# Kernel optimization log

Hardware: AMD Instinct MI355X
Metric: run time of the kernel (lower is better)

Reference implementation:

```python
import jax, jax.numpy as jnp
import numpy as np

B, S, C, H = 256, 512, 64, 128  # batch, seq_len, input channels, LSTM hidden


def setup_inputs() -> dict:
    key = jax.random.key(0)
    ks = jax.random.split(key, 9)
    s = 1.0 / np.sqrt(H)  # torch nn.LSTM init: U(-1/sqrt(H), 1/sqrt(H))
    u = lambda k, shape: jax.random.uniform(k, shape, jnp.float32, -s, s)
    return {
        "x": jax.random.normal(ks[0], (B, S, C), jnp.float32),
        # layer 0 (input size C)
        "Wih0": u(ks[1], (4 * H, C)),
        "Whh0": u(ks[2], (4 * H, H)),
        "bih0": u(ks[3], (4 * H,)),
        "bhh0": u(ks[4], (4 * H,)),
        # layer 1 (input size H)
        "Wih1": u(ks[5], (4 * H, H)),
        "Whh1": u(ks[6], (4 * H, H)),
        "bih1": u(ks[7], (4 * H,)),
        "bhh1": u(ks[8], (4 * H,)),
    }


def _lstm_layer(x, Wih, Whh, bih, bhh):
    """x: (S, B, in) -> outputs h_t for all t: (S, B, H). Torch gate order i,f,g,o."""
    Hh = Whh.shape[1]
    # Input-to-hidden GEMM hoisted out of the recurrence (batched over S).
    xg = jnp.einsum('sbc,gc->sbg', x, Wih) + bih + bhh  # (S, B, 4H)

    def step(carry, xt):
        h, c = carry
        g = xt + h @ Whh.T  # (B, 4H)
        i, f, gg, o = jnp.split(g, 4, axis=-1)
        i = jax.nn.sigmoid(i)
        f = jax.nn.sigmoid(f)
        gg = jnp.tanh(gg)
        o = jax.nn.sigmoid(o)
        c = f * c + i * gg
        h = o * jnp.tanh(c)
        return (h, c), h

    h0 = jnp.zeros((x.shape[1], Hh), x.dtype)
    _, ys = jax.lax.scan(step, (h0, h0), xg)
    return ys


def reference(x, Wih0, Whh0, bih0, bhh0, Wih1, Whh1, bih1, bhh1):
    xs = jnp.transpose(x, (1, 0, 2))  # (B,S,C) -> (S,B,C), matching x.permute(1,0,2)
    y1 = _lstm_layer(xs, Wih0, Whh0, bih0, bhh0)
    y2 = _lstm_layer(y1, Wih1, Whh1, bih1, bhh1)
    return y2[-1]  # x[-1, :, :]: last timestep of top layer, (B, H)
```

## Files before the change

kernel.cpp:

```cpp
#include <hip/hip_runtime.h>
#include <cstdint>
#include <cstddef>


#define S_LEN 512
#define B_SZ  256
#define C_IN  64
#define HDIM  128
#define NBLK  64
#define XG_TSTRIDE (64 * 512 * 4)

using short4v = __attribute__((ext_vector_type(4))) short;
using short8  = __attribute__((ext_vector_type(8))) short;
using float4v = __attribute__((ext_vector_type(4))) float;

template<bool V> struct Flag { static constexpr bool value = V; };

__device__ __forceinline__ unsigned short f2b(float f) {
    union { float f; unsigned int u; } v; v.f = f;
    unsigned int u = v.u;
    return (unsigned short)((u + 0x7FFFu + ((u >> 16) & 1u)) >> 16);
}
__device__ __forceinline__ float b2f(unsigned short s) {
    union { unsigned int u; float f; } v; v.u = ((unsigned int)s) << 16;
    return v.f;
}
__device__ __forceinline__ float sig_(float x) {
    return __builtin_amdgcn_rcpf(1.0f + __builtin_amdgcn_exp2f(x * -1.442695041f));
}
__device__ __forceinline__ float tanh_(float x) {
    return 1.0f - 2.0f * __builtin_amdgcn_rcpf(1.0f + __builtin_amdgcn_exp2f(x * 2.885390082f));
}
__device__ __forceinline__ short8 load8_f2b(const float* s) {
    const float4v f0 = *(const float4v*)s;
    const float4v f1 = *(const float4v*)(s + 4);
    short8 t;
#pragma unroll
    for (int e = 0; e < 4; ++e) {
        t[e]     = (short)f2b(f0[e]);
        t[e + 4] = (short)f2b(f1[e]);
    }
    return t;
}

__global__ void conv_kernel(const float* __restrict__ whh0,
                            const float* __restrict__ wih1, const float* __restrict__ whh1,
                            const float* __restrict__ bih1, const float* __restrict__ bhh1,
                            unsigned short* __restrict__ whh0_b, unsigned short* __restrict__ wih1_b,
                            unsigned short* __restrict__ whh1_b, float* __restrict__ bias1) {
    int i = blockIdx.x * blockDim.x + threadIdx.x;
    if (i < 4 * HDIM * HDIM) {
        whh0_b[i] = f2b(whh0[i]);
        wih1_b[i] = f2b(wih1[i]);
        whh1_b[i] = f2b(whh1[i]);
    }
    if (i < 4 * HDIM) bias1[i] = bih1[i] + bhh1[i];
}

__global__ __launch_bounds__(512, 2)
void xg_gemm(const float* __restrict__ x, const float* __restrict__ wih0,
             const float* __restrict__ bih0, const float* __restrict__ bhh0,
             unsigned short* __restrict__ xg) {
    const int tid = threadIdx.x;
    const int w = tid >> 6, L = tid & 63, q = L >> 4, r = L & 15;
    const int blk = blockIdx.x, tch = blockIdx.y;
    const int boff = blk * 4, j = w * 16 + r;
    const int rowload = r >> 2;

    short8 wf[4][2]; float bias_s[4];
#pragma unroll
    for (int g = 0; g < 4; ++g) {
        const int nrow = g * HDIM + j;
#pragma unroll
        for (int kk = 0; kk < 2; ++kk)
            wf[g][kk] = load8_f2b(wih0 + (size_t)nrow * C_IN + kk * 32 + q * 8);
        bias_s[g] = bih0[nrow] + bhh0[nrow];
    }

    const float* px = x + ((size_t)(boff + rowload) * S_LEN + (size_t)tch * 32) * C_IN + q * 8;
    unsigned short* po = xg + ((size_t)(tch * 32) * NBLK + blk) * 2048 + (size_t)tid * 4;

    for (int tt = 0; tt < 32; ++tt) {
        short8 xa[2];
#pragma unroll
        for (int kk = 0; kk < 2; ++kk) xa[kk] = load8_f2b(px + kk * 32);
        float4v a[4];
#pragma unroll
        for (int g = 0; g < 4; ++g) a[g] = (float4v){bias_s[g], 0.f, 0.f, 0.f};
#pragma unroll
        for (int kk = 0; kk < 2; ++kk)
#pragma unroll
            for (int g = 0; g < 4; ++g)
                a[g] = __builtin_amdgcn_mfma_f32_16x16x32_bf16(xa[kk], wf[g][kk], a[g], 0, 0, 0);
        short4v o;
#pragma unroll
        for (int g = 0; g < 4; ++g) o[g] = (short)f2b(a[g][0]);
        *(short4v*)po = o;
        px += C_IN;
        po += XG_TSTRIDE;
    }
}

__global__ __launch_bounds__(512, 2)
void lstm_fused(const unsigned short* __restrict__ whh0_b,
                const unsigned short* __restrict__ wih1_b,
                const unsigned short* __restrict__ whh1_b,
                const float* __restrict__ bias1,
                const unsigned short* __restrict__ xg,
                float* __restrict__ out) {
    __shared__ __align__(16) unsigned short hbuf[4 * 2048];
    const int tid = threadIdx.x;
    const int w = tid >> 6, L = tid & 63, q = L >> 4, r = L & 15;
    const int blk = blockIdx.x;
    const int boff = blk * 4, j = w * 16 + r;

    short8 whh0[4][4], wih1[4][4], whh1[4][4];
    float b1s[4];
#pragma unroll
    for (int g = 0; g < 4; ++g) {
        const size_t nrow = (size_t)(g * HDIM + j);
#pragma unroll
        for (int kk = 0; kk < 4; ++kk) {
            whh0[g][kk] = *(const short8*)(whh0_b + nrow * HDIM + kk * 32 + q * 8);
            wih1[g][kk] = *(const short8*)(wih1_b + nrow * HDIM + kk * 32 + q * 8);
            whh1[g][kk] = *(const short8*)(whh1_b + nrow * HDIM + kk * 32 + q * 8);
        }
        b1s[g] = bias1[g * HDIM + j];
    }
#pragma unroll
    for (int g = 0; g < 4; ++g) {
        asm volatile("" : "+v"(whh0[g][0]), "+v"(whh0[g][1]), "+v"(whh0[g][2]), "+v"(whh0[g][3]));
        asm volatile("" : "+v"(wih1[g][0]), "+v"(wih1[g][1]), "+v"(wih1[g][2]), "+v"(wih1[g][3]));
        asm volatile("" : "+v"(whh1[g][0]), "+v"(whh1[g][1]), "+v"(whh1[g][2]), "+v"(whh1[g][3]));
    }

    for (int idx = tid; idx < 4 * 1024; idx += 512) ((unsigned int*)hbuf)[idx] = 0u;

    float cf0 = 0.f, cf1 = 0.f;
    const int rred = r & ~3;
    const int rdoff = q * 128 + rred * 8;
    const int chunkbase = (j >> 3) * 128 + (j & 7);
    const int wslot = chunkbase + (4 * q) * 8;
    float* fout = out + (size_t)(boff + q) * HDIM + j;

    const unsigned short* pxg = xg + (size_t)blk * 2048 + (size_t)tid * 4;
    short4v xgA = *(const short4v*)pxg;
    pxg += XG_TSTRIDE;
    short4v xgB;

    __syncthreads();

    auto step = [&](auto D0_, auto D1_, auto FIN_,
                    unsigned short* r0, unsigned short* w0,
                    unsigned short* r1, unsigned short* w1,
                    short4v& xc, short4v& xn) {
        constexpr bool D0  = decltype(D0_)::value;
        constexpr bool D1  = decltype(D1_)::value;
        constexpr bool FIN = decltype(FIN_)::value;

        if constexpr (!FIN) {
            xn = *(const short4v*)pxg;
            pxg += XG_TSTRIDE;
        }

        if constexpr (D0) {
            float4v a0[4];
#pragma unroll
            for (int g = 0; g < 4; ++g)
                a0[g] = (float4v){b2f((unsigned short)xc[g]), 0.f, 0.f, 0.f};
            __builtin_amdgcn_s_setprio(1);
#pragma unroll
            for (int kk = 0; kk < 4; ++kk) {
                const short8 h0f = *(const short8*)(r0 + kk * 512 + rdoff);
#pragma unroll
                for (int g = 0; g < 4; ++g)
                    a0[g] = __builtin_amdgcn_mfma_f32_16x16x32_bf16(h0f, whh0[g][kk], a0[g], 0, 0, 0);
            }
            __builtin_amdgcn_s_setprio(0);
            {
                const float iv = sig_(a0[0][0]);
                const float fv = sig_(a0[1][0]);
                const float gv = tanh_(a0[2][0]);
                const float ov = sig_(a0[3][0]);
                cf0 = fv * cf0 + iv * gv;
                w0[wslot] = f2b(ov * tanh_(cf0));
            }
        }

        if constexpr (D1) {
            float4v a1[4];
#pragma unroll
            for (int g = 0; g < 4; ++g) a1[g] = (float4v){b1s[g], 0.f, 0.f, 0.f};
            __builtin_amdgcn_s_setprio(1);
#pragma unroll
            for (int kk = 0; kk < 4; ++kk) {
                const short8 hif = *(const short8*)(r0 + kk * 512 + rdoff);
#pragma unroll
                for (int g = 0; g < 4; ++g)
                    a1[g] = __builtin_amdgcn_mfma_f32_16x16x32_bf16(hif, wih1[g][kk], a1[g], 0, 0, 0);
            }
#pragma unroll
            for (int kk = 0; kk < 4; ++kk) {
                const short8 h1f = *(const short8*)(r1 + kk * 512 + rdoff);
#pragma unroll
                for (int g = 0; g < 4; ++g)
                    a1[g] = __builtin_amdgcn_mfma_f32_16x16x32_bf16(h1f, whh1[g][kk], a1[g], 0, 0, 0);
            }
            __builtin_amdgcn_s_setprio(0);
            {
                const float iv = sig_(a1[0][0]);
                const float fv = sig_(a1[1][0]);
                const float gv = tanh_(a1[2][0]);
                const float ov = sig_(a1[3][0]);
                cf1 = fv * cf1 + iv * gv;
                const float hv = ov * tanh_(cf1);
                if constexpr (FIN) fout[0] = hv;
                else w1[wslot] = f2b(hv);
            }
        }

        if constexpr (!FIN)
            asm volatile("s_waitcnt lgkmcnt(0)\n\ts_barrier" ::: "memory");
    };

    unsigned short* h0A = hbuf;
    unsigned short* h0B = hbuf + 2048;
    unsigned short* h1A = hbuf + 4096;
    unsigned short* h1B = hbuf + 6144;
    using T = Flag<true>; using F = Flag<false>;

    step(T{}, F{}, F{}, h0A, h0B, h1A, h1B, xgA, xgB);
#pragma unroll 1
    for (int k = 0; k < 255; ++k) {
        step(T{}, T{}, F{}, h0B, h0A, h1B, h1A, xgB, xgA);
        step(T{}, T{}, F{}, h0A, h0B, h1A, h1B, xgA, xgB);
    }
    step(T{}, T{}, F{}, h0B, h0A, h1B, h1A, xgB, xgA);
    step(F{}, T{}, T{}, h0A, h0B, h1A, h1B, xgA, xgB);
}


extern "C" void kernel_launch(void* const* d_in, const int* in_sizes, int n_in,
                              void* d_out, int out_size, void* d_ws, size_t ws_size,
                              hipStream_t stream) {
    const float* x    = (const float*)d_in[0];
    const float* wih0 = (const float*)d_in[1];
    const float* whh0 = (const float*)d_in[2];
    const float* bih0 = (const float*)d_in[3];
    const float* bhh0 = (const float*)d_in[4];
    const float* wih1 = (const float*)d_in[5];
    const float* whh1 = (const float*)d_in[6];
    const float* bih1 = (const float*)d_in[7];
    const float* bhh1 = (const float*)d_in[8];

    char* ws = (char*)d_ws;
    unsigned short* whh0_b = (unsigned short*)(ws + 0);
    unsigned short* wih1_b = (unsigned short*)(ws + 131072);
    unsigned short* whh1_b = (unsigned short*)(ws + 262144);
    float*          bias1  = (float*)(ws + 393216);
    unsigned short* xgp    = (unsigned short*)(ws + 524288);

    conv_kernel<<<256, 256, 0, stream>>>(whh0, wih1, whh1, bih1, bhh1,
                                         whh0_b, wih1_b, whh1_b, bias1);
    xg_gemm<<<dim3(NBLK, 16), 512, 0, stream>>>(x, wih0, bih0, bhh0, xgp);
    lstm_fused<<<NBLK, 512, 0, stream>>>(whh0_b, wih1_b, whh1_b, bias1, xgp,
                                         (float*)d_out);
}
```

Before: 694.5 us.

## Fuse weight conversion into LSTM kernel, densify xg GEMM, stagger layer order across waves

Measured after the change: 758.7 us. 1.09x slower.

```diff
diff --git a/kernel.cpp b/kernel.cpp
--- a/kernel.cpp
+++ b/kernel.cpp
@@ -41,20 +41,6 @@
         t[e + 4] = (short)f2b(f1[e]);
     }
     return t;
-}
-
-__global__ void conv_kernel(const float* __restrict__ whh0,
-                            const float* __restrict__ wih1, const float* __restrict__ whh1,
-                            const float* __restrict__ bih1, const float* __restrict__ bhh1,
-                            unsigned short* __restrict__ whh0_b, unsigned short* __restrict__ wih1_b,
-                            unsigned short* __restrict__ whh1_b, float* __restrict__ bias1) {
-    int i = blockIdx.x * blockDim.x + threadIdx.x;
-    if (i < 4 * HDIM * HDIM) {
-        whh0_b[i] = f2b(whh0[i]);
-        wih1_b[i] = f2b(wih1[i]);
-        whh1_b[i] = f2b(whh1[i]);
-    }
-    if (i < 4 * HDIM) bias1[i] = bih1[i] + bhh1[i];
 }
 
 __global__ __launch_bounds__(512, 2)
@@ -65,7 +51,6 @@
     const int w = tid >> 6, L = tid & 63, q = L >> 4, r = L & 15;
     const int blk = blockIdx.x, tch = blockIdx.y;
     const int boff = blk * 4, j = w * 16 + r;
-    const int rowload = r >> 2;
 
     short8 wf[4][2]; float bias_s[4];
 #pragma unroll
@@ -77,35 +62,40 @@
         bias_s[g] = bih0[nrow] + bhh0[nrow];
     }
 
-    const float* px = x + ((size_t)(boff + rowload) * S_LEN + (size_t)tch * 32) * C_IN + q * 8;
-    unsigned short* po = xg + ((size_t)(tch * 32) * NBLK + blk) * 2048 + (size_t)tid * 4;
-
-    for (int tt = 0; tt < 32; ++tt) {
+    const float* px = x + ((size_t)(boff + (r & 3)) * S_LEN + tch * 16 + (r >> 2)) * C_IN;
+
+#pragma unroll
+    for (int tb = 0; tb < 4; ++tb) {
+        const float* pa = px + (size_t)(tb * 4) * C_IN;
         short8 xa[2];
 #pragma unroll
-        for (int kk = 0; kk < 2; ++kk) xa[kk] = load8_f2b(px + kk * 32);
+        for (int kk = 0; kk < 2; ++kk) xa[kk] = load8_f2b(pa + kk * 32 + q * 8);
         float4v a[4];
 #pragma unroll
-        for (int g = 0; g < 4; ++g) a[g] = (float4v){bias_s[g], 0.f, 0.f, 0.f};
+        for (int g = 0; g < 4; ++g)
+            a[g] = (float4v){bias_s[g], bias_s[g], bias_s[g], bias_s[g]};
 #pragma unroll
         for (int kk = 0; kk < 2; ++kk)
 #pragma unroll
             for (int g = 0; g < 4; ++g)
                 a[g] = __builtin_amdgcn_mfma_f32_16x16x32_bf16(xa[kk], wf[g][kk], a[g], 0, 0, 0);
-        short4v o;
-#pragma unroll
-        for (int g = 0; g < 4; ++g) o[g] = (short)f2b(a[g][0]);
-        *(short4v*)po = o;
-        px += C_IN;
-        po += XG_TSTRIDE;
+        const size_t obase = ((size_t)(tch * 16 + tb * 4 + q) * NBLK + blk) * 2048
+                             + (size_t)(w * 64 + r) * 4;
+#pragma unroll
+        for (int e = 0; e < 4; ++e) {
+            short4v o;
+#pragma unroll
+            for (int g = 0; g < 4; ++g) o[g] = (short)f2b(a[g][e]);
+            *(short4v*)(xg + obase + e * 64) = o;
+        }
     }
 }
 
 __global__ __launch_bounds__(512, 2)
-void lstm_fused(const unsigned short* __restrict__ whh0_b,
-                const unsigned short* __restrict__ wih1_b,
-                const unsigned short* __restrict__ whh1_b,
-                const float* __restrict__ bias1,
+void lstm_fused(const float* __restrict__ whh0_f,
+                const float* __restrict__ wih1_f,
+                const float* __restrict__ whh1_f,
+                const float* __restrict__ bih1, const float* __restrict__ bhh1,
                 const unsigned short* __restrict__ xg,
                 float* __restrict__ out) {
     __shared__ __align__(16) unsigned short hbuf[4 * 2048];
@@ -121,17 +111,17 @@
         const size_t nrow = (size_t)(g * HDIM + j);
 #pragma unroll
         for (int kk = 0; kk < 4; ++kk) {
-            whh0[g][kk] = *(const short8*)(whh0_b + nrow * HDIM + kk * 32 + q * 8);
-            wih1[g][kk] = *(const short8*)(wih1_b + nrow * HDIM + kk * 32 + q * 8);
-            whh1[g][kk] = *(const short8*)(whh1_b + nrow * HDIM + kk * 32 + q * 8);
-        }
-        b1s[g] = bias1[g * HDIM + j];
+            whh0[g][kk] = load8_f2b(whh0_f + nrow * HDIM + kk * 32 + q * 8);
+            wih1[g][kk] = load8_f2b(wih1_f + nrow * HDIM + kk * 32 + q * 8);
+            whh1[g][kk] = load8_f2b(whh1_f + nrow * HDIM + kk * 32 + q * 8);
+        }
+        b1s[g] = bih1[nrow] + bhh1[nrow];
     }
 #pragma unroll
     for (int g = 0; g < 4; ++g) {
-        asm volatile("" : "+v"(whh0[g][0]), "+v"(whh0[g][1]), "+v"(whh0[g][2]), "+v"(whh0[g][3]));
-        asm volatile("" : "+v"(wih1[g][0]), "+v"(wih1[g][1]), "+v"(wih1[g][2]), "+v"(wih1[g][3]));
-        asm volatile("" : "+v"(whh1[g][0]), "+v"(whh1[g][1]), "+v"(whh1[g][2]), "+v"(whh1[g][3]));
+        asm volatile("" : "+a"(whh0[g][0]), "+a"(whh0[g][1]), "+a"(whh0[g][2]), "+a"(whh0[g][3]));
+        asm volatile("" : "+a"(wih1[g][0]), "+a"(wih1[g][1]), "+a"(wih1[g][2]), "+a"(wih1[g][3]));
+        asm volatile("" : "+a"(whh1[g][0]), "+a"(whh1[g][1]), "+a"(whh1[g][2]), "+a"(whh1[g][3]));
     }
 
     for (int idx = tid; idx < 4 * 1024; idx += 512) ((unsigned int*)hbuf)[idx] = 0u;
@@ -149,6 +139,58 @@
     short4v xgB;
 
     __syncthreads();
+
+    auto doL0 = [&](unsigned short* r0, unsigned short* w0, short4v& xc) {
+        float4v a0[4];
+#pragma unroll
+        for (int g = 0; g < 4; ++g)
+            a0[g] = (float4v){b2f((unsigned short)xc[g]), 0.f, 0.f, 0.f};
+        __builtin_amdgcn_s_setprio(1);
+#pragma unroll
+        for (int kk = 0; kk < 4; ++kk) {
+            const short8 h0f = *(const short8*)(r0 + kk * 512 + rdoff);
+#pragma unroll
+            for (int g = 0; g < 4; ++g)
+                a0[g] = __builtin_amdgcn_mfma_f32_16x16x32_bf16(h0f, whh0[g][kk], a0[g], 0, 0, 0);
+        }
+        __builtin_amdgcn_s_setprio(0);
+        const float iv = sig_(a0[0][0]);
+        const float fv = sig_(a0[1][0]);
+        const float gv = tanh_(a0[2][0]);
+        const float ov = sig_(a0[3][0]);
+        cf0 = fv * cf0 + iv * gv;
+        w0[wslot] = f2b(ov * tanh_(cf0));
+    };
+    auto doL1 = [&](unsigned short* r0, unsigned short* r1, unsigned short* w1, auto FIN_) {
+        constexpr bool FIN = decltype(FIN_)::value;
+        float4v a1[4];
+#pragma unroll
+        for (int g = 0; g < 4; ++g) a1[g] = (float4v){b1s[g], 0.f, 0.f, 0.f};
+        __builtin_amdgcn_s_setprio(1);
+#pragma unroll
+        for (int kk = 0; kk < 4; ++kk) {
+            const short8 hif = *(const short8*)(r0 + kk * 512 + rdoff);
+#pragma unroll
+            for (int g = 0; g < 4; ++g)
+                a1[g] = __builtin_amdgcn_mfma_f32_16x16x32_bf16(hif, wih1[g][kk], a1[g], 0, 0, 0);
+        }
+#pragma unroll
+        for (int kk = 0; kk < 4; ++kk) {
+            const short8 h1f = *(const short8*)(r1 + kk * 512 + rdoff);
+#pragma unroll
+            for (int g = 0; g < 4; ++g)
+                a1[g] = __builtin_amdgcn_mfma_f32_16x16x32_bf16(h1f, whh1[g][kk], a1[g], 0, 0, 0);
+        }
+        __builtin_amdgcn_s_setprio(0);
+        const float iv = sig_(a1[0][0]);
+        const float fv = sig_(a1[1][0]);
+        const float gv = tanh_(a1[2][0]);
+        const float ov = sig_(a1[3][0]);
+        cf1 = fv * cf1 + iv * gv;
+        const float hv = ov * tanh_(cf1);
+        if constexpr (FIN) fout[0] = hv;
+        else w1[wslot] = f2b(hv);
+    };
 
     auto step = [&](auto D0_, auto D1_, auto FIN_,
                     unsigned short* r0, unsigned short* w0,
@@ -163,60 +205,17 @@
             pxg += XG_TSTRIDE;
         }
 
-        if constexpr (D0) {
-            float4v a0[4];
-#pragma unroll
-            for (int g = 0; g < 4; ++g)
-                a0[g] = (float4v){b2f((unsigned short)xc[g]), 0.f, 0.f, 0.f};
-            __builtin_amdgcn_s_setprio(1);
-#pragma unroll
-            for (int kk = 0; kk < 4; ++kk) {
-                const short8 h0f = *(const short8*)(r0 + kk * 512 + rdoff);
-#pragma unroll
-                for (int g = 0; g < 4; ++g)
-                    a0[g] = __builtin_amdgcn_mfma_f32_16x16x32_bf16(h0f, whh0[g][kk], a0[g], 0, 0, 0);
+        if constexpr (D0 && D1) {
+            if (w & 4) {
+                doL1(r0, r1, w1, FIN_);
+                doL0(r0, w0, xc);
+            } else {
+                doL0(r0, w0, xc);
+                doL1(r0, r1, w1, FIN_);
             }
-            __builtin_amdgcn_s_setprio(0);
-            {
-                const float iv = sig_(a0[0][0]);
-                const float fv = sig_(a0[1][0]);
-                const float gv = tanh_(a0[2][0]);
-                const float ov = sig_(a0[3][0]);
-                cf0 = fv * cf0 + iv * gv;
-                w0[wslot] = f2b(ov * tanh_(cf0));
-            }
-        }
-
-        if constexpr (D1) {
-            float4v a1[4];
-#pragma unroll
-            for (int g = 0; g < 4; ++g) a1[g] = (float4v){b1s[g], 0.f, 0.f, 0.f};
-            __builtin_amdgcn_s_setprio(1);
-#pragma unroll
-            for (int kk = 0; kk < 4; ++kk) {
-                const short8 hif = *(const short8*)(r0 + kk * 512 + rdoff);
-#pragma unroll
-                for (int g = 0; g < 4; ++g)
-                    a1[g] = __builtin_amdgcn_mfma_f32_16x16x32_bf16(hif, wih1[g][kk], a1[g], 0, 0, 0);
-            }
-#pragma unroll
-            for (int kk = 0; kk < 4; ++kk) {
-                const short8 h1f = *(const short8*)(r1 + kk * 512 + rdoff);
-#pragma unroll
-                for (int g = 0; g < 4; ++g)
-                    a1[g] = __builtin_amdgcn_mfma_f32_16x16x32_bf16(h1f, whh1[g][kk], a1[g], 0, 0, 0);
-            }
-            __builtin_amdgcn_s_setprio(0);
-            {
-                const float iv = sig_(a1[0][0]);
-                const float fv = sig_(a1[1][0]);
-                const float gv = tanh_(a1[2][0]);
-                const float ov = sig_(a1[3][0]);
-                cf1 = fv * cf1 + iv * gv;
-                const float hv = ov * tanh_(cf1);
-                if constexpr (FIN) fout[0] = hv;
-                else w1[wslot] = f2b(hv);
-            }
+        } else {
+            if constexpr (D0) doL0(r0, w0, xc);
+            if constexpr (D1) doL1(r0, r1, w1, FIN_);
         }
 
         if constexpr (!FIN)
@@ -253,16 +252,9 @@
     const float* bih1 = (const float*)d_in[7];
     const float* bhh1 = (const float*)d_in[8];
 
-    char* ws = (char*)d_ws;
-    unsigned short* whh0_b = (unsigned short*)(ws + 0);
-    unsigned short* wih1_b = (unsigned short*)(ws + 131072);
-    unsigned short* whh1_b = (unsigned short*)(ws + 262144);
-    float*          bias1  = (float*)(ws + 393216);
-    unsigned short* xgp    = (unsigned short*)(ws + 524288);
-
-    conv_kernel<<<256, 256, 0, stream>>>(whh0, wih1, whh1, bih1, bhh1,
-                                         whh0_b, wih1_b, whh1_b, bias1);
-    xg_gemm<<<dim3(NBLK, 16), 512, 0, stream>>>(x, wih0, bih0, bhh0, xgp);
-    lstm_fused<<<NBLK, 512, 0, stream>>>(whh0_b, wih1_b, whh1_b, bias1, xgp,
+    unsigned short* xgp = (unsigned short*)d_ws;
+
+    xg_gemm<<<dim3(NBLK, 32), 512, 0, stream>>>(x, wih0, bih0, bhh0, xgp);
+    lstm_fused<<<NBLK, 512, 0, stream>>>(whh0, wih1, whh1, bih1, bhh1, xgp,
                                          (float*)d_out);
 }
```
